# Kernel optimization log

Measured on AMD Instinct MI355X. Metric: run time of the kernel, lower is better.

## Reference

```python
import jax, jax.numpy as jnp
import numpy as np

SHARPNESS = 1000.0   # sigmoid temperature from source: *1000.0
BIAS = 0.008         # shadow acne bias from source: -0.008
FILTER_SIZE = 1      # 3x3 PCF
SHADOW_STEP = 1


def setup_inputs() -> dict:
    key = jax.random.key(0)
    k1, k2, k3 = jax.random.split(key, 3)
    N, H, W, K, S = 8, 1024, 1024, 1, 2048
    # light-view depth buffer (fragments_from_light.zbuf), K=1 squeezed
    light_zbuf = jax.random.uniform(k1, (N, S, S), dtype=jnp.float32)
    depth_z = jax.random.uniform(k2, (N, H, W, K), dtype=jnp.float32)
    # rounded integer light-screen coords per camera pixel: [..., 0]=x, [..., 1]=y
    xy = jax.random.randint(k3, (N, H, W, K, 2), 0, S, dtype=jnp.int32)
    return {"light_zbuf": light_zbuf, "depth_z": depth_z, "xy": xy, "image_size": S}


def reference(light_zbuf, depth_z, xy, image_size):
    N, H, W, K = depth_z.shape
    b = jnp.arange(N, dtype=jnp.int32)[:, None, None, None]  # broadcast batch index
    x = xy[..., 0]  # [N,H,W,K]
    y = xy[..., 1]
    aa = depth_z - BIAS
    vis = jnp.zeros_like(depth_z)
    # 3x3 PCF: gather clamped neighbors in the light zbuf, soft depth test, accumulate
    for ii in range(-FILTER_SIZE, FILTER_SIZE + 1):
        for jj in range(-FILTER_SIZE, FILTER_SIZE + 1):
            yi = jnp.clip(y + ii * SHADOW_STEP, 0, image_size - 1)
            xi = jnp.clip(x + jj * SHADOW_STEP, 0, image_size - 1)
            bb = light_zbuf[b, yi, xi]  # [N,H,W,K] gather
            vis = vis + jax.nn.sigmoid((bb - aa) * SHARPNESS)
    return vis / float((1 + 2 * FILTER_SIZE) ** 2)
```

## Files before the change

kernel.cpp:

```cpp
#include <hip/hip_runtime.h>


#define SHARPNESS 1000.0f
#define BIAS 0.008f

#define S_IMG   2048
#define NBATCH  8
#define HWK     (1 << 20)
#define TSHIFT  8
#define NTILES  8
#define PPB     4096
#define NTHR    512
#define NBLOCKS ((NBATCH * HWK) / PPB)
#define CPB     (HWK / PPB)

typedef float f4u __attribute__((ext_vector_type(4), aligned(4)));
typedef int   i4v __attribute__((ext_vector_type(4)));

__device__ __forceinline__ float sigf(float bb, float a) {
    return 1.0f / (1.0f + __expf((a - bb) * SHARPNESS));
}
__device__ __forceinline__ float selv(f4u v, int s) {
    return (s == 0) ? v.x : (s == 1) ? v.y : (s == 2) ? v.z : v.w;
}

struct G9 { f4u v0, v1, v2; int x; };

__device__ __forceinline__ void g9_issue(G9& g, const float* __restrict__ zb,
                                         unsigned rec, int t) {
    const int x  = (int)((rec >> 12) & 0x7FFu);
    const int y  = (t << TSHIFT) | (int)(rec >> 23);
    const int ym = (y > 0) ? y - 1 : 0;
    const int yp = (y < S_IMG - 1) ? y + 1 : S_IMG - 1;
    const int xb = min(max(x - 1, 0), S_IMG - 4);
    const float* base = zb + xb;
    g.v0 = *(const f4u*)(base + (size_t)ym * S_IMG);
    g.v1 = *(const f4u*)(base + (size_t)y  * S_IMG);
    g.v2 = *(const f4u*)(base + (size_t)yp * S_IMG);
    g.x  = x;
}

__device__ __forceinline__ float g9_eval(const G9& g, float a) {
    if (g.x >= 1 && g.x <= S_IMG - 3) {
        return sigf(g.v0.x, a) + sigf(g.v0.y, a) + sigf(g.v0.z, a)
             + sigf(g.v1.x, a) + sigf(g.v1.y, a) + sigf(g.v1.z, a)
             + sigf(g.v2.x, a) + sigf(g.v2.y, a) + sigf(g.v2.z, a);
    } else {
        const int xb = min(max(g.x - 1, 0), S_IMG - 4);
        const int s0 = max(g.x - 1, 0) - xb;
        const int s1 = g.x - xb;
        const int s2 = min(g.x + 1, S_IMG - 1) - xb;
        return sigf(selv(g.v0, s0), a) + sigf(selv(g.v0, s1), a) + sigf(selv(g.v0, s2), a)
             + sigf(selv(g.v1, s0), a) + sigf(selv(g.v1, s1), a) + sigf(selv(g.v1, s2), a)
             + sigf(selv(g.v2, s0), a) + sigf(selv(g.v2, s1), a) + sigf(selv(g.v2, s2), a);
    }
}

__global__ __launch_bounds__(NTHR, 8) void pcf_fused(
    const float* __restrict__ zbuf, const float* __restrict__ depth,
    const int* __restrict__ xy_raw, float* __restrict__ out)
{
    __shared__ float    sd[PPB];
    __shared__ unsigned srec[PPB];
    __shared__ unsigned cnt[NTILES];
    __shared__ unsigned cur[NTILES];
    __shared__ unsigned seg[NTILES + 1];

    const int g   = blockIdx.x;
    const int b   = g & (NBATCH - 1);
    const int c   = g >> 3;
    const int tid = threadIdx.x;
    const int blk = b * CPB + c;
    const size_t pbase = (size_t)blk * PPB;
    const float* zb = zbuf + (size_t)b * ((size_t)S_IMG * S_IMG);

    if (tid < NTILES) cnt[tid] = 0;
    __syncthreads();

    unsigned rloc[8];
    unsigned tpack = 0;
    const i4v* xy4 = (const i4v*)(xy_raw + 2 * pbase);
#pragma unroll
    for (int j = 0; j < 4; ++j) {
        const i4v q = __builtin_nontemporal_load(&xy4[j * NTHR + tid]);
        const int il0 = (j * NTHR + tid) * 2;
        const int t0  = q.y >> TSHIFT;
        const int t1  = q.w >> TSHIFT;
        rloc[2 * j]     = (unsigned)il0
                        | ((unsigned)q.x << 12)
                        | ((unsigned)(q.y & ((1 << TSHIFT) - 1)) << 23);
        rloc[2 * j + 1] = (unsigned)(il0 + 1)
                        | ((unsigned)q.z << 12)
                        | ((unsigned)(q.w & ((1 << TSHIFT) - 1)) << 23);
        tpack |= ((unsigned)t0 << (6 * j)) | ((unsigned)t1 << (6 * j + 3));
        atomicAdd(&cnt[t0], 1u);
        atomicAdd(&cnt[t1], 1u);
    }
    const f4u* dw = (const f4u*)(depth + pbase);
#pragma unroll
    for (int j = 0; j < PPB / (NTHR * 4); ++j)
        ((f4u*)sd)[j * NTHR + tid] = __builtin_nontemporal_load(&dw[j * NTHR + tid]);
    __syncthreads();

    if (tid == 0) {
        unsigned s = 0;
#pragma unroll
        for (int t = 0; t < NTILES; ++t) { seg[t] = s; cur[t] = s; s += cnt[t]; }
        seg[NTILES] = s;
    }
    __syncthreads();
#pragma unroll
    for (int j = 0; j < 8; ++j) {
        const int t = (int)((tpack >> (3 * j)) & 7u);
        const unsigned pos = atomicAdd(&cur[t], 1u);
        srec[pos] = rloc[j];
    }
    __syncthreads();

    const int e1 = (int)seg[1], e2 = (int)seg[2], e3 = (int)seg[3],
              e4 = (int)seg[4], e5 = (int)seg[5], e6 = (int)seg[6],
              e7 = (int)seg[7];
#define TILE8(k) ((int)((k) >= e1) + (int)((k) >= e2) + (int)((k) >= e3) + \
                  (int)((k) >= e4) + (int)((k) >= e5) + (int)((k) >= e6) + \
                  (int)((k) >= e7))

    {
        unsigned recA = srec[tid];
        int  ilA = (int)(recA & 0xFFFu);
        G9 gA; g9_issue(gA, zb, recA, TILE8(tid));
        float aA = sd[ilA] - BIAS;
#pragma unroll
        for (int i = 0; i < PPB / NTHR - 1; ++i) {
            const int kB = (i + 1) * NTHR + tid;
            const unsigned recB = srec[kB];
            const int  ilB = (int)(recB & 0xFFFu);
            G9 gB; g9_issue(gB, zb, recB, TILE8(kB));
            const float aB = sd[ilB] - BIAS;
            __builtin_amdgcn_sched_barrier(0);
            sd[ilA] = g9_eval(gA, aA) * (1.0f / 9.0f);
            gA = gB; aA = aB; ilA = ilB;
        }
        sd[ilA] = g9_eval(gA, aA) * (1.0f / 9.0f);
    }
    __syncthreads();

    f4u* ow = (f4u*)(out + pbase);
#pragma unroll
    for (int j = 0; j < PPB / (NTHR * 4); ++j)
        __builtin_nontemporal_store(((const f4u*)sd)[j * NTHR + tid], &ow[j * NTHR + tid]);
#undef TILE8
}

__global__ __launch_bounds__(256) void pcf_shadow_generic(
    const float* __restrict__ zbuf, const float* __restrict__ depth_z,
    const int2* __restrict__ xy, const int* __restrict__ image_size_p,
    float* __restrict__ out, int total, int zbuf_elems)
{
    const int i = blockIdx.x * blockDim.x + threadIdx.x;
    if (i >= total) return;
    const int S  = *image_size_p;
    const int SS = S * S;
    const int N  = zbuf_elems / SS;
    const int hwk = total / N;
    const int b   = i / hwk;
    const float a = depth_z[i] - BIAS;
    const int2 p  = xy[i];
    const float* base = zbuf + (size_t)b * (size_t)SS;
    float vis = 0.0f;
#pragma unroll
    for (int ii = -1; ii <= 1; ++ii) {
        const int yi = min(max(p.y + ii, 0), S - 1);
        const float* row = base + (size_t)yi * (size_t)S;
#pragma unroll
        for (int jj = -1; jj <= 1; ++jj) {
            const int xi = min(max(p.x + jj, 0), S - 1);
            vis += 1.0f / (1.0f + __expf((a - row[xi]) * SHARPNESS));
        }
    }
    out[i] = vis * (1.0f / 9.0f);
}

extern "C" void kernel_launch(void* const* d_in, const int* in_sizes, int n_in,
                              void* d_out, int out_size, void* d_ws, size_t ws_size,
                              hipStream_t stream) {
    const float* zbuf     = (const float*)d_in[0];
    const float* depth_z  = (const float*)d_in[1];
    const int*   xy_raw   = (const int*)d_in[2];
    const int*   img_size = (const int*)d_in[3];
    float*       out      = (float*)d_out;

    const int zbuf_elems = in_sizes[0];
    const int total      = in_sizes[1];

    if (zbuf_elems == NBATCH * S_IMG * S_IMG && total == NBATCH * HWK) {
        pcf_fused<<<NBLOCKS, NTHR, 0, stream>>>(zbuf, depth_z, xy_raw, out);
    } else {
        const int block = 256;
        const int grid  = (total + block - 1) / block;
        pcf_shadow_generic<<<grid, block, 0, stream>>>(zbuf, depth_z, (const int2*)xy_raw,
                                                       img_size, out, total, zbuf_elems);
    }
}
```

Baseline: 466.1 us.

## Issue all gathers up front per thread and use exp2/rcp sigmoid

New measurement: 498.1 us. 1.07x slower.

```diff
diff --git a/kernel.cpp b/kernel.cpp
--- a/kernel.cpp
+++ b/kernel.cpp
@@ -3,6 +3,7 @@
 
 #define SHARPNESS 1000.0f
 #define BIAS 0.008f
+#define S2LOG2E 1442.6950408889634f
 
 #define S_IMG   2048
 #define NBATCH  8
@@ -11,6 +12,7 @@
 #define NTILES  8
 #define PPB     4096
 #define NTHR    512
+#define RPT     (PPB / NTHR)
 #define NBLOCKS ((NBATCH * HWK) / PPB)
 #define CPB     (HWK / PPB)
 
@@ -18,7 +20,8 @@
 typedef int   i4v __attribute__((ext_vector_type(4)));
 
 __device__ __forceinline__ float sigf(float bb, float a) {
-    return 1.0f / (1.0f + __expf((a - bb) * SHARPNESS));
+    const float t = (a - bb) * S2LOG2E;
+    return __builtin_amdgcn_rcpf(1.0f + exp2f(t));
 }
 __device__ __forceinline__ float selv(f4u v, int s) {
     return (s == 0) ? v.x : (s == 1) ? v.y : (s == 2) ? v.z : v.w;
@@ -56,7 +59,7 @@
     }
 }
 
-__global__ __launch_bounds__(NTHR, 8) void pcf_fused(
+__global__ __launch_bounds__(NTHR, 4) void pcf_fused(
     const float* __restrict__ zbuf, const float* __restrict__ depth,
     const int* __restrict__ xy_raw, float* __restrict__ out)
 {
@@ -77,11 +80,11 @@
     if (tid < NTILES) cnt[tid] = 0;
     __syncthreads();
 
-    unsigned rloc[8];
+    unsigned rloc[RPT];
     unsigned tpack = 0;
     const i4v* xy4 = (const i4v*)(xy_raw + 2 * pbase);
 #pragma unroll
-    for (int j = 0; j < 4; ++j) {
+    for (int j = 0; j < RPT / 2; ++j) {
         const i4v q = __builtin_nontemporal_load(&xy4[j * NTHR + tid]);
         const int il0 = (j * NTHR + tid) * 2;
         const int t0  = q.y >> TSHIFT;
@@ -110,7 +113,7 @@
     }
     __syncthreads();
 #pragma unroll
-    for (int j = 0; j < 8; ++j) {
+    for (int j = 0; j < RPT; ++j) {
         const int t = (int)((tpack >> (3 * j)) & 7u);
         const unsigned pos = atomicAdd(&cur[t], 1u);
         srec[pos] = rloc[j];
@@ -125,22 +128,19 @@
                   (int)((k) >= e7))
 
     {
-        unsigned recA = srec[tid];
-        int  ilA = (int)(recA & 0xFFFu);
-        G9 gA; g9_issue(gA, zb, recA, TILE8(tid));
-        float aA = sd[ilA] - BIAS;
-#pragma unroll
-        for (int i = 0; i < PPB / NTHR - 1; ++i) {
-            const int kB = (i + 1) * NTHR + tid;
-            const unsigned recB = srec[kB];
-            const int  ilB = (int)(recB & 0xFFFu);
-            G9 gB; g9_issue(gB, zb, recB, TILE8(kB));
-            const float aB = sd[ilB] - BIAS;
-            __builtin_amdgcn_sched_barrier(0);
-            sd[ilA] = g9_eval(gA, aA) * (1.0f / 9.0f);
-            gA = gB; aA = aB; ilA = ilB;
-        }
-        sd[ilA] = g9_eval(gA, aA) * (1.0f / 9.0f);
+        unsigned recv[RPT]; int ilv[RPT]; float av[RPT]; G9 gg[RPT];
+#pragma unroll
+        for (int i = 0; i < RPT; ++i) recv[i] = srec[i * NTHR + tid];
+#pragma unroll
+        for (int i = 0; i < RPT; ++i) ilv[i] = (int)(recv[i] & 0xFFFu);
+#pragma unroll
+        for (int i = 0; i < RPT; ++i) av[i] = sd[ilv[i]] - BIAS;
+#pragma unroll
+        for (int i = 0; i < RPT; ++i)
+            g9_issue(gg[i], zb, recv[i], TILE8(i * NTHR + tid));
+#pragma unroll
+        for (int i = 0; i < RPT; ++i)
+            sd[ilv[i]] = g9_eval(gg[i], av[i]) * (1.0f / 9.0f);
     }
     __syncthreads();
 
```
